# Kernel optimization log

Measured on AMD Instinct MI355X. Metric: run time of the kernel, lower is better.

Reference implementation:

```python
import jax, jax.numpy as jnp
import numpy as np
import math

B, S, D, H = 2, 2048, 1024, 16
DK = D // H


def setup_inputs() -> dict:
    key = jax.random.key(0)
    ks = jax.random.split(key, 12)
    s = 1.0 / math.sqrt(D)
    inp = {
        "q": jax.random.normal(ks[0], (B, S, D), jnp.float32),
        "k": jax.random.normal(ks[1], (B, S, D), jnp.float32),
        "v": jax.random.normal(ks[2], (B, S, D), jnp.float32),
        "mask": jnp.broadcast_to(jnp.tril(jnp.ones((S, S), jnp.int32))[None, None], (B, 1, S, S)),
        "Wq": jax.random.normal(ks[3], (D, D), jnp.float32) * s,
        "bq": jnp.zeros((D,), jnp.float32),
        "Wk": jax.random.normal(ks[4], (D, D), jnp.float32) * s,
        "bk": jnp.zeros((D,), jnp.float32),
        "Wv": jax.random.normal(ks[5], (D, D), jnp.float32) * s,
        "bv": jnp.zeros((D,), jnp.float32),
        "Wo": jax.random.normal(ks[6], (D, D), jnp.float32) * s,
        "bo": jnp.zeros((D,), jnp.float32),
    }
    return inp


def reference(q, k, v, mask, Wq, bq, Wk, bk, Wv, bv, Wo, bo):
    b = q.shape[0]
    # project and split heads -> [b, h, s, d_k]
    def heads(x, W, bias):
        y = x @ W.T + bias
        return y.reshape(b, -1, H, DK).transpose(0, 2, 1, 3)
    qh = heads(q, Wq, bq)
    kh = heads(k, Wk, bk)
    vh = heads(v, Wv, bv)
    scores = jnp.einsum("bhqd,bhkd->bhqk", qh, kh) / math.sqrt(DK)
    scores = jnp.where(mask == 0, jnp.float32(-1e9), scores)
    weights = jax.nn.softmax(scores, axis=-1)  # dropout p=0 -> identity
    out = jnp.einsum("bhqk,bhkd->bhqd", weights, vh)
    out = out.transpose(0, 2, 1, 3).reshape(b, -1, H * DK)
    return out @ Wo.T + bo
```

## Files before the change

kernel.cpp:

```cpp
#include <hip/hip_runtime.h>

#define B_ 2
#define S_ 2048
#define D_ 1024
#define H_ 16
#define DK_ 64
#define M_ 4096

typedef unsigned short u16;
typedef __bf16 bf16x8 __attribute__((ext_vector_type(8)));
typedef float floatx4 __attribute__((ext_vector_type(4)));

#if __has_builtin(__builtin_amdgcn_exp2f)
#define EXP2F(x) __builtin_amdgcn_exp2f(x)
#else
#define EXP2F(x) exp2f(x)
#endif

__device__ __forceinline__ u16 f2bf(float f) {
  unsigned u = __float_as_uint(f);
  u += 0x7fffu + ((u >> 16) & 1u);
  return (u16)(u >> 16);
}

__device__ __forceinline__ void stage16(const void* g, void* l) {
  __builtin_amdgcn_global_load_lds(
      (const __attribute__((address_space(1))) unsigned int*)g,
      (__attribute__((address_space(3))) unsigned int*)l, 16, 0, 0);
}

__global__ __launch_bounds__(256) void cvt_all_kernel(
    const float* __restrict__ q, const float* __restrict__ k, const float* __restrict__ v,
    const float* __restrict__ wq, const float* __restrict__ wk,
    const float* __restrict__ wv, const float* __restrict__ wo,
    u16* dq, u16* dk, u16* dv, u16* dwq, u16* dwk, u16* dwv, u16* dwo) {
  const float* s; u16* d; size_t base;
  const int bx = blockIdx.x;
  if (bx < 6144) {
    const int t0 = bx >> 11;
    base = (size_t)(bx & 2047) * 2048;
    s = t0 == 0 ? q : t0 == 1 ? k : v;
    d = t0 == 0 ? dq : t0 == 1 ? dk : dv;
  } else {
    const int t0 = (bx - 6144) >> 9;
    base = (size_t)((bx - 6144) & 511) * 2048;
    s = t0 == 0 ? wq : t0 == 1 ? wk : t0 == 2 ? wv : wo;
    d = t0 == 0 ? dwq : t0 == 1 ? dwk : t0 == 2 ? dwv : dwo;
  }
  const size_t i = base + (size_t)threadIdx.x * 8;
  const float4 f0 = *reinterpret_cast<const float4*>(s + i);
  const float4 f1 = *reinterpret_cast<const float4*>(s + i + 4);
  union { u16 h[8]; uint4 u; } cv;
  cv.h[0] = f2bf(f0.x); cv.h[1] = f2bf(f0.y); cv.h[2] = f2bf(f0.z); cv.h[3] = f2bf(f0.w);
  cv.h[4] = f2bf(f1.x); cv.h[5] = f2bf(f1.y); cv.h[6] = f2bf(f1.z); cv.h[7] = f2bf(f1.w);
  *reinterpret_cast<uint4*>(d + i) = cv.u;
}

template <int BN>
__device__ __forceinline__ void gemm_body(
    const u16* __restrict__ A, const u16* __restrict__ W,
    const float* __restrict__ bias, void* __restrict__ outp,
    int mode, float scale) {
  constexpr int NT = BN / 32;
  constexpr int NBI = BN / 64;
  __shared__ __align__(16) u16 As[2][128 * 32];
  __shared__ __align__(16) u16 Bs[2][BN * 32];

  const int t = threadIdx.x;
  const int lane = t & 63, w = t >> 6;
  const int quad = lane >> 4, l16 = lane & 15;
  const int wm = w >> 1, wn = w & 1;
  const int m0 = blockIdx.x * 128, n0 = blockIdx.y * BN;

  const int sp = lane >> 3, ssw = lane & 7, sc = ssw ^ sp;
  const u16 *gA[2], *gB[NBI]; u16 *lA[2], *lB[NBI];
#pragma unroll
  for (int i = 0; i < 2; i++) {
    const int ri = i * 4 + w;
    gA[i] = A + (size_t)(m0 + ri * 16 + 2 * sp + (sc >> 2)) * 1024 + (sc & 3) * 8;
    lA[i] = As[0] + ri * 64 * 8;
  }
#pragma unroll
  for (int i = 0; i < NBI; i++) {
    const int ri = i * 4 + w;
    gB[i] = W + (size_t)(n0 + ri * 16 + 2 * sp + (sc >> 2)) * 1024 + (sc & 3) * 8;
    lB[i] = Bs[0] + ri * 64 * 8;
  }

  floatx4 acc[4][NT] = {};

#pragma unroll
  for (int i = 0; i < 2; i++) stage16(gA[i], lA[i]);
#pragma unroll
  for (int i = 0; i < NBI; i++) stage16(gB[i], lB[i]);

  for (int k0 = 0; k0 < 1024; k0 += 32) {
    const int cur = (k0 >> 5) & 1, nxt = cur ^ 1;
    __syncthreads();
    if (k0 + 32 < 1024) {
#pragma unroll
      for (int i = 0; i < 2; i++) stage16(gA[i] + k0 + 32, lA[i] + nxt * 128 * 32);
#pragma unroll
      for (int i = 0; i < NBI; i++) stage16(gB[i] + k0 + 32, lB[i] + nxt * BN * 32);
    }
    bf16x8 af[4], bf[NT];
#pragma unroll
    for (int mt = 0; mt < 4; mt++) {
      const int row = wm * 64 + mt * 16 + l16;
      const int pg = row >> 1;
      const int sw = (((row & 1) << 2) | quad) ^ (pg & 7);
      af[mt] = *reinterpret_cast<const bf16x8*>(&As[cur][(pg * 8 + sw) * 8]);
    }
#pragma unroll
    for (int nt = 0; nt < NT; nt++) {
      const int row = wn * (NT * 16) + nt * 16 + l16;
      const int pg = row >> 1;
      const int sw = (((row & 1) << 2) | quad) ^ (pg & 7);
      bf[nt] = *reinterpret_cast<const bf16x8*>(&Bs[cur][(pg * 8 + sw) * 8]);
    }
#pragma unroll
    for (int mt = 0; mt < 4; mt++)
#pragma unroll
      for (int nt = 0; nt < NT; nt++)
        acc[mt][nt] = __builtin_amdgcn_mfma_f32_16x16x32_bf16(af[mt], bf[nt], acc[mt][nt], 0, 0, 0);
  }

#pragma unroll
  for (int mt = 0; mt < 4; mt++) {
    const int mbase = m0 + wm * 64 + mt * 16 + quad * 4;
    const int bb = mbase >> 11, s0v = mbase & 2047;
#pragma unroll
    for (int nt = 0; nt < NT; nt++) {
      const int n = n0 + wn * (NT * 16) + nt * 16 + l16;
      const float bvv = bias[n];
      if (mode == 0) {
        u16* Y = (u16*)outp;
        const int h = n >> 6, dk = n & 63;
#pragma unroll
        for (int r = 0; r < 4; r++)
          Y[(((size_t)(bb * H_ + h)) * S_ + (s0v + r)) * DK_ + dk] =
              f2bf((acc[mt][nt][r] + bvv) * scale);
      } else if (mode == 2) {
        u16* Y = (u16*)outp;
        const int h = n >> 6, dk = n & 63;
        union { u16 h4[4]; uint2 u; } pk2;
#pragma unroll
        for (int r = 0; r < 4; r++) pk2.h4[r] = f2bf(acc[mt][nt][r] + bvv);
        *reinterpret_cast<uint2*>(
            &Y[(((size_t)(bb * H_ + h)) * DK_ + dk) * S_ + s0v]) = pk2.u;
      } else {
        float* Y = (float*)outp;
#pragma unroll
        for (int r = 0; r < 4; r++)
          Y[(size_t)(mbase + r) * 1024 + n] = acc[mt][nt][r] + bvv;
      }
    }
  }
}

__global__ __launch_bounds__(256) void qkv_gemm_kernel(
    const u16* qa, const u16* ka, const u16* va,
    const u16* wq, const u16* wk, const u16* wv,
    const float* bq, const float* bk, const float* bv,
    u16* Qh, u16* Kh, u16* VhT) {
  const int g = blockIdx.z;
  const u16* A = g == 0 ? qa : g == 1 ? ka : va;
  const u16* W = g == 0 ? wq : g == 1 ? wk : wv;
  const float* bias = g == 0 ? bq : g == 1 ? bk : bv;
  void* out = g == 0 ? (void*)Qh : g == 1 ? (void*)Kh : (void*)VhT;
  gemm_body<128>(A, W, bias, out, g == 2 ? 2 : 0,
                 g == 0 ? 0.18033688011112f : 1.0f);
}

__global__ __launch_bounds__(256) void o_gemm_kernel(
    const u16* ctx, const u16* wo, const float* bo, float* out) {
  gemm_body<64>(ctx, wo, bo, out, 3, 1.0f);
}

__global__ __launch_bounds__(256) void attn_kernel(
    const u16* __restrict__ Qh, const u16* __restrict__ Kh,
    const u16* __restrict__ VhT, u16* __restrict__ Ctx) {
  __shared__ __align__(16) u16 Kt[2][64 * 64];
  __shared__ __align__(16) u16 Vt[2][64 * 64];
  __shared__ __align__(16) u16 Ps[64 * 72];

  const int t = threadIdx.x;
  const int lane = t & 63, w = t >> 6;
  const int quad = lane >> 4, l16 = lane & 15;

  const int bh = blockIdx.x & 31;
  const int i = blockIdx.x >> 5;
  const int j = i >> 3, r0 = i & 7;
  const int u = (j == 0) ? 31 - r0 : (j == 1) ? r0 : (j == 2) ? 23 - r0 : 8 + r0;
  const int qb = u * 64;
  const int ntile = u + 1;

  const u16* Qp = Qh + (size_t)bh * S_ * DK_;
  const u16* Kp = Kh + (size_t)bh * S_ * DK_;
  const u16* Vp = VhT + (size_t)bh * DK_ * S_;

  bf16x8 bq[2];
#pragma unroll
  for (int kk = 0; kk < 2; kk++)
    bq[kk] = *reinterpret_cast<const bf16x8*>(
        &Qp[(size_t)(qb + w * 16 + l16) * DK_ + kk * 32 + quad * 8]);

  const u16 *gK[2], *gV[2]; u16 *lK[2], *lV[2];
#pragma unroll
  for (int i2 = 0; i2 < 2; i2++) {
    const int ch = (i2 * 4 + w) * 64 + lane;
    const int row = ch >> 3, c = ch & 7, cs = c ^ (row & 7);
    gK[i2] = Kp + (size_t)row * DK_ + cs * 8;
    gV[i2] = Vp + (size_t)row * S_ + cs * 8;
    lK[i2] = Kt[0] + ((i2 * 4 + w) * 64) * 8;
    lV[i2] = Vt[0] + ((i2 * 4 + w) * 64) * 8;
  }

  float l_run = 0.f;
  floatx4 o[4] = {};
  const int qg = qb + w * 16 + l16;

#pragma unroll
  for (int i2 = 0; i2 < 2; i2++) {
    stage16(gK[i2], lK[i2]);
    stage16(gV[i2], lV[i2]);
  }

  for (int it = 0; it < ntile; it++) {
    const int cur = it & 1, nxt = cur ^ 1;
    __syncthreads();
    if (it + 1 < ntile) {
      const int j1 = (it + 1) * 64;
#pragma unroll
      for (int i2 = 0; i2 < 2; i2++) {
        stage16(gK[i2] + (size_t)j1 * DK_, lK[i2] + nxt * 64 * 64);
        stage16(gV[i2] + j1, lV[i2] + nxt * 64 * 64);
      }
    }
    const int j0 = it * 64;

    floatx4 sc[4] = {};
#pragma unroll
    for (int mt = 0; mt < 4; mt++) {
      const int row = mt * 16 + l16;
#pragma unroll
      for (int kk = 0; kk < 2; kk++) {
        const bf16x8 ak = *reinterpret_cast<const bf16x8*>(
            &Kt[cur][(row * 8 + ((kk * 4 + quad) ^ (l16 & 7))) * 8]);
        sc[mt] = __builtin_amdgcn_mfma_f32_16x16x32_bf16(ak, bq[kk], sc[mt], 0, 0, 0);
      }
    }

    const bool maskT = (it == ntile - 1);
    float psum = 0.f;
#pragma unroll
    for (int mt = 0; mt < 4; mt++) {
      float p[4];
#pragma unroll
      for (int r = 0; r < 4; r++) {
        float vsc = sc[mt][r];
        if (maskT && (j0 + mt * 16 + quad * 4 + r > qg)) vsc = -1e30f;
        p[r] = EXP2F(vsc);
        psum += p[r];
      }
      uint2 pu;
      pu.x = (__float_as_uint(p[1]) & 0xffff0000u) | (__float_as_uint(p[0]) >> 16);
      pu.y = (__float_as_uint(p[3]) & 0xffff0000u) | (__float_as_uint(p[2]) >> 16);
      *reinterpret_cast<uint2*>(&Ps[(w * 16 + l16) * 72 + mt * 16 + quad * 4]) = pu;
    }
    psum += __shfl_xor(psum, 16);
    psum += __shfl_xor(psum, 32);
    l_run += psum;

#pragma unroll
    for (int kk = 0; kk < 2; kk++) {
      const bf16x8 ap = *reinterpret_cast<const bf16x8*>(
          &Ps[(w * 16 + l16) * 72 + kk * 32 + quad * 8]);
#pragma unroll
      for (int nt = 0; nt < 4; nt++) {
        const bf16x8 bv = *reinterpret_cast<const bf16x8*>(
            &Vt[cur][((nt * 16 + l16) * 8 + ((kk * 4 + quad) ^ (l16 & 7))) * 8]);
        o[nt] = __builtin_amdgcn_mfma_f32_16x16x32_bf16(ap, bv, o[nt], 0, 0, 0);
      }
    }
  }

  const int bb = bh >> 4, hh = bh & 15;
#pragma unroll
  for (int r = 0; r < 4; r++) {
    const float lr = __shfl(l_run, quad * 4 + r);
    const float inv = 1.0f / lr;
    const int srow = qb + w * 16 + quad * 4 + r;
    u16* cp = Ctx + ((size_t)bb * S_ + srow) * D_ + hh * DK_;
#pragma unroll
    for (int nt = 0; nt < 4; nt++)
      cp[nt * 16 + l16] = f2bf(o[nt][r] * inv);
  }
}

extern "C" void kernel_launch(void* const* d_in, const int* in_sizes, int n_in,
                              void* d_out, int out_size, void* d_ws, size_t ws_size,
                              hipStream_t stream) {
  const float* q  = (const float*)d_in[0];
  const float* k  = (const float*)d_in[1];
  const float* v  = (const float*)d_in[2];
  const float* Wq = (const float*)d_in[4];
  const float* bq = (const float*)d_in[5];
  const float* Wk = (const float*)d_in[6];
  const float* bk = (const float*)d_in[7];
  const float* Wv = (const float*)d_in[8];
  const float* bv = (const float*)d_in[9];
  const float* Wo = (const float*)d_in[10];
  const float* bo = (const float*)d_in[11];

  const size_t nW = (size_t)D_ * D_;
  const size_t nA = (size_t)M_ * D_;
  u16* wqb = (u16*)d_ws;
  u16* wkb = wqb + nW;
  u16* wvb = wkb + nW;
  u16* wob = wvb + nW;
  u16* qb_ = wob + nW;
  u16* kb_ = qb_ + nA;
  u16* vb_ = kb_ + nA;
  u16* Qh  = vb_ + nA;
  u16* Kh  = Qh + nA;
  u16* VhT = Kh + nA;
  u16* Ctx = qb_;

  cvt_all_kernel<<<dim3(8192), 256, 0, stream>>>(q, k, v, Wq, Wk, Wv, Wo,
                                                 qb_, kb_, vb_, wqb, wkb, wvb, wob);

  qkv_gemm_kernel<<<dim3(M_ / 128, D_ / 128, 3), 256, 0, stream>>>(
      qb_, kb_, vb_, wqb, wkb, wvb, bq, bk, bv, Qh, Kh, VhT);

  attn_kernel<<<dim3(B_ * H_ * (S_ / 64)), 256, 0, stream>>>(Qh, Kh, VhT, Ctx);

  o_gemm_kernel<<<dim3(M_ / 128, D_ / 64), 256, 0, stream>>>(Ctx, wob, bo, (float*)d_out);
}
```

Before: 241.3 us.

## Split attention key tile across warp pairs and skip fully masked diagonal subtile

Changes the work split in the attention kernel. Each warp now handles 32 query rows against half of the 64-key tile, where before it handled 16 query rows against the full tile. Each K and V fragment read from LDS therefore feeds two MFMAs. On the diagonal tile, the warp whose key half lies wholly above its query rows skips the tile. Partial outputs and row sums from the two key halves are combined through shared memory at the end, which adds an epilogue barrier and extra LDS traffic, and leaves half the warps idle during the final store.

```diff
diff --git a/kernel.cpp b/kernel.cpp
--- a/kernel.cpp
+++ b/kernel.cpp
@@ -187,6 +187,9 @@
   const int t = threadIdx.x;
   const int lane = t & 63, w = t >> 6;
   const int quad = lane >> 4, l16 = lane & 15;
+  const int qpair = w & 1;
+  const int shalf = w >> 1;
+  const int s_off = shalf * 32;
 
   const int bh = blockIdx.x & 31;
   const int i = blockIdx.x >> 5;
@@ -199,11 +202,13 @@
   const u16* Kp = Kh + (size_t)bh * S_ * DK_;
   const u16* Vp = VhT + (size_t)bh * DK_ * S_;
 
-  bf16x8 bq[2];
-#pragma unroll
-  for (int kk = 0; kk < 2; kk++)
-    bq[kk] = *reinterpret_cast<const bf16x8*>(
-        &Qp[(size_t)(qb + w * 16 + l16) * DK_ + kk * 32 + quad * 8]);
+  bf16x8 bq[2][2];
+#pragma unroll
+  for (int g = 0; g < 2; g++)
+#pragma unroll
+    for (int kk = 0; kk < 2; kk++)
+      bq[g][kk] = *reinterpret_cast<const bf16x8*>(
+          &Qp[(size_t)(qb + qpair * 32 + g * 16 + l16) * DK_ + kk * 32 + quad * 8]);
 
   const u16 *gK[2], *gV[2]; u16 *lK[2], *lV[2];
 #pragma unroll
@@ -216,9 +221,8 @@
     lV[i2] = Vt[0] + ((i2 * 4 + w) * 64) * 8;
   }
 
-  float l_run = 0.f;
-  floatx4 o[4] = {};
-  const int qg = qb + w * 16 + l16;
+  float l_run[2] = {0.f, 0.f};
+  floatx4 o[2][4] = {};
 
 #pragma unroll
   for (int i2 = 0; i2 < 2; i2++) {
@@ -238,63 +242,99 @@
       }
     }
     const int j0 = it * 64;
-
-    floatx4 sc[4] = {};
-#pragma unroll
-    for (int mt = 0; mt < 4; mt++) {
-      const int row = mt * 16 + l16;
+    const bool diag = (it == ntile - 1);
+    if (diag && qpair == 0 && shalf == 1) continue;
+
+    floatx4 sc[2][2] = {};
+#pragma unroll
+    for (int mt = 0; mt < 2; mt++) {
+      const int row = s_off + mt * 16 + l16;
 #pragma unroll
       for (int kk = 0; kk < 2; kk++) {
         const bf16x8 ak = *reinterpret_cast<const bf16x8*>(
             &Kt[cur][(row * 8 + ((kk * 4 + quad) ^ (l16 & 7))) * 8]);
-        sc[mt] = __builtin_amdgcn_mfma_f32_16x16x32_bf16(ak, bq[kk], sc[mt], 0, 0, 0);
-      }
-    }
-
-    const bool maskT = (it == ntile - 1);
-    float psum = 0.f;
-#pragma unroll
-    for (int mt = 0; mt < 4; mt++) {
-      float p[4];
+        sc[0][mt] = __builtin_amdgcn_mfma_f32_16x16x32_bf16(ak, bq[0][kk], sc[0][mt], 0, 0, 0);
+        sc[1][mt] = __builtin_amdgcn_mfma_f32_16x16x32_bf16(ak, bq[1][kk], sc[1][mt], 0, 0, 0);
+      }
+    }
+
+    const bool needMask = diag && (qpair <= shalf);
+#pragma unroll
+    for (int g = 0; g < 2; g++) {
+      const int qg = qb + qpair * 32 + g * 16 + l16;
+      float psum = 0.f;
+#pragma unroll
+      for (int mt = 0; mt < 2; mt++) {
+        float p[4];
+#pragma unroll
+        for (int r = 0; r < 4; r++) {
+          float vsc = sc[g][mt][r];
+          if (needMask && (j0 + s_off + mt * 16 + quad * 4 + r > qg)) vsc = -1e30f;
+          p[r] = EXP2F(vsc);
+          psum += p[r];
+        }
+        uint2 pu;
+        pu.x = (__float_as_uint(p[1]) & 0xffff0000u) | (__float_as_uint(p[0]) >> 16);
+        pu.y = (__float_as_uint(p[3]) & 0xffff0000u) | (__float_as_uint(p[2]) >> 16);
+        *reinterpret_cast<uint2*>(
+            &Ps[(qpair * 32 + g * 16 + l16) * 72 + s_off + mt * 16 + quad * 4]) = pu;
+      }
+      psum += __shfl_xor(psum, 16);
+      psum += __shfl_xor(psum, 32);
+      l_run[g] += psum;
+    }
+
+    bf16x8 ap[2];
+#pragma unroll
+    for (int g = 0; g < 2; g++)
+      ap[g] = *reinterpret_cast<const bf16x8*>(
+          &Ps[(qpair * 32 + g * 16 + l16) * 72 + s_off + quad * 8]);
+#pragma unroll
+    for (int nt = 0; nt < 4; nt++) {
+      const bf16x8 bv = *reinterpret_cast<const bf16x8*>(
+          &Vt[cur][((nt * 16 + l16) * 8 + ((shalf * 4 + quad) ^ (l16 & 7))) * 8]);
+      o[0][nt] = __builtin_amdgcn_mfma_f32_16x16x32_bf16(ap[0], bv, o[0][nt], 0, 0, 0);
+      o[1][nt] = __builtin_amdgcn_mfma_f32_16x16x32_bf16(ap[1], bv, o[1][nt], 0, 0, 0);
+    }
+  }
+
+  __syncthreads();
+  float* ocomb = (float*)Kt;
+  float* lcomb = (float*)Vt;
+  if (shalf == 1) {
+#pragma unroll
+    for (int g = 0; g < 2; g++)
+#pragma unroll
+      for (int nt = 0; nt < 4; nt++)
+        *reinterpret_cast<floatx4*>(
+            &ocomb[((qpair * 8 + g * 4 + nt) * 64 + lane) * 4]) = o[g][nt];
+    lcomb[qpair * 128 + lane * 2 + 0] = l_run[0];
+    lcomb[qpair * 128 + lane * 2 + 1] = l_run[1];
+  }
+  __syncthreads();
+  if (shalf == 0) {
+#pragma unroll
+    for (int g = 0; g < 2; g++)
+#pragma unroll
+      for (int nt = 0; nt < 4; nt++)
+        o[g][nt] += *reinterpret_cast<const floatx4*>(
+            &ocomb[((qpair * 8 + g * 4 + nt) * 64 + lane) * 4]);
+    l_run[0] += lcomb[qpair * 128 + lane * 2 + 0];
+    l_run[1] += lcomb[qpair * 128 + lane * 2 + 1];
+
+    const int bb = bh >> 4, hh = bh & 15;
+#pragma unroll
+    for (int g = 0; g < 2; g++)
 #pragma unroll
       for (int r = 0; r < 4; r++) {
-        float vsc = sc[mt][r];
-        if (maskT && (j0 + mt * 16 + quad * 4 + r > qg)) vsc = -1e30f;
-        p[r] = EXP2F(vsc);
-        psum += p[r];
-      }
-      uint2 pu;
-      pu.x = (__float_as_uint(p[1]) & 0xffff0000u) | (__float_as_uint(p[0]) >> 16);
-      pu.y = (__float_as_uint(p[3]) & 0xffff0000u) | (__float_as_uint(p[2]) >> 16);
-      *reinterpret_cast<uint2*>(&Ps[(w * 16 + l16) * 72 + mt * 16 + quad * 4]) = pu;
-    }
-    psum += __shfl_xor(psum, 16);
-    psum += __shfl_xor(psum, 32);
-    l_run += psum;
-
-#pragma unroll
-    for (int kk = 0; kk < 2; kk++) {
-      const bf16x8 ap = *reinterpret_cast<const bf16x8*>(
-          &Ps[(w * 16 + l16) * 72 + kk * 32 + quad * 8]);
-#pragma unroll
-      for (int nt = 0; nt < 4; nt++) {
-        const bf16x8 bv = *reinterpret_cast<const bf16x8*>(
-            &Vt[cur][((nt * 16 + l16) * 8 + ((kk * 4 + quad) ^ (l16 & 7))) * 8]);
-        o[nt] = __builtin_amdgcn_mfma_f32_16x16x32_bf16(ap, bv, o[nt], 0, 0, 0);
-      }
-    }
-  }
-
-  const int bb = bh >> 4, hh = bh & 15;
-#pragma unroll
-  for (int r = 0; r < 4; r++) {
-    const float lr = __shfl(l_run, quad * 4 + r);
-    const float inv = 1.0f / lr;
-    const int srow = qb + w * 16 + quad * 4 + r;
-    u16* cp = Ctx + ((size_t)bb * S_ + srow) * D_ + hh * DK_;
-#pragma unroll
-    for (int nt = 0; nt < 4; nt++)
-      cp[nt * 16 + l16] = f2bf(o[nt][r] * inv);
+        const float lr = __shfl(l_run[g], quad * 4 + r);
+        const float inv = 1.0f / lr;
+        const int srow = qb + qpair * 32 + g * 16 + quad * 4 + r;
+        u16* cp = Ctx + ((size_t)bb * S_ + srow) * D_ + hh * DK_;
+#pragma unroll
+        for (int nt = 0; nt < 4; nt++)
+          cp[nt * 16 + l16] = f2bf(o[g][nt][r] * inv);
+      }
   }
 }
 
```

Measured after the change: 246.6 us. +2.2%, slower.
